# Optimization experiments

Measured on AMD Instinct MI355X. Metric: run time of the kernel, lower is better.

## Reference

```python
import jax, jax.numpy as jnp
import numpy as np

NUM_SAMPLES = 64
HIDDEN = 256
BATCH = 16384


def setup_inputs() -> dict:
    key = jax.random.key(0)
    ks = jax.random.split(key, 12)
    origins = jax.random.normal(ks[0], (BATCH, 3), dtype=jnp.float32)
    directions = jax.random.normal(ks[1], (BATCH, 3), dtype=jnp.float32)
    directions = directions / jnp.linalg.norm(directions, axis=-1, keepdims=True)

    def init_linear(k, fan_in, fan_out):
        kw, kb = jax.random.split(k)
        lim = 1.0 / np.sqrt(fan_in)
        W = jax.random.uniform(kw, (fan_in, fan_out), jnp.float32, -lim, lim)
        b = jax.random.uniform(kb, (fan_out,), jnp.float32, -lim, lim)
        return W, b

    W1, b1 = init_linear(ks[2], 3, HIDDEN)
    W2, b2 = init_linear(ks[3], HIDDEN, HIDDEN)
    W3, b3 = init_linear(ks[4], HIDDEN, HIDDEN)
    W4, b4 = init_linear(ks[5], HIDDEN, 4)
    return {
        "origins": origins, "directions": directions,
        "W1": W1, "b1": b1, "W2": W2, "b2": b2,
        "W3": W3, "b3": b3, "W4": W4, "b4": b4,
        "near": 2, "far": 6,
    }


def _field(points, W1, b1, W2, b2, W3, b3, W4, b4):
    # points: [N, 3] -> [N, 4] (rgb logits + density logit)
    h = jax.nn.relu(points @ W1 + b1)
    h = jax.nn.relu(h @ W2 + b2)
    h = jax.nn.relu(h @ W3 + b3)
    return h @ W4 + b4


def reference(origins, directions, W1, b1, W2, b2, W3, b3, W4, b4, near, far):
    near = jnp.float32(near)
    far = jnp.float32(far)
    B = origins.shape[0]
    S = NUM_SAMPLES

    # 1. Stratified (uniform midpoint) samples along each ray.
    t_vals = jnp.linspace(0.0, 1.0, S + 1, dtype=jnp.float32)      # [S+1]
    z_vals = near * (1.0 - t_vals) + far * t_vals                   # [S+1]
    boundaries = jnp.broadcast_to(z_vals, (B, S + 1))               # [B, S+1]
    z_mids = 0.5 * (z_vals[:-1] + z_vals[1:])                       # [S]
    points = origins[:, None, :] + directions[:, None, :] * z_mids[None, :, None]  # [B, S, 3]

    # 2. Evaluate field; map channels to valid ranges.
    outputs = _field(points.reshape(-1, 3), W1, b1, W2, b2, W3, b3, W4, b4)
    outputs = outputs.reshape(B, S, 4)
    emitted_radiance = jax.nn.sigmoid(outputs[..., :3])             # [B, S, 3]
    density = jax.nn.relu(outputs[..., 3])                          # [B, S]

    # 3. Alpha values from densities and segment lengths.
    deltas = boundaries[:, 1:] - boundaries[:, :-1]                 # [B, S]
    alphas = 1.0 - jnp.exp(-density * deltas)                       # [B, S]

    # 4. Alpha compositing (black background).
    trans = jnp.cumprod(
        jnp.concatenate([jnp.ones((B, 1), jnp.float32), 1.0 - alphas + 1e-10], axis=-1),
        axis=-1,
    )[:, :-1]                                                        # [B, S]
    weights = alphas * trans                                         # [B, S]
    rgb = jnp.sum(weights[..., None] * emitted_radiance, axis=1)     # [B, 3]
    return rgb
```

## Files before the change

### kernel.cpp

```cpp
#include <hip/hip_runtime.h>


#define HID 256

typedef short bf16x8 __attribute__((ext_vector_type(8)));
typedef float f32x4  __attribute__((ext_vector_type(4)));
typedef float f32x16 __attribute__((ext_vector_type(16)));
typedef int   i32x4  __attribute__((ext_vector_type(4)));
typedef int   i32x2v __attribute__((ext_vector_type(2)));

static __device__ __forceinline__ unsigned short f2bf(float f) {
    unsigned u = __float_as_uint(f);
    u += 0x7fffu + ((u >> 16) & 1u);
    return (unsigned short)(u >> 16);
}

__global__ void prep_pack(const float* __restrict__ W2, const float* __restrict__ W3,
                          const float* __restrict__ W4,
                          unsigned short* __restrict__ W2p, unsigned short* __restrict__ W3p,
                          unsigned short* __restrict__ W4p) {
    int t = blockIdx.x * 256 + threadIdx.x;
    if (t < 65536) {
        int e  = t & 7;
        int l  = (t >> 3) & 63;
        int kt = (t >> 9) & 15;
        int nt = t >> 13;
        int k = kt * 16 + 8 * (l >> 5) + e;
        int n = nt * 32 + (l & 31);
        W2p[t] = f2bf(W2[k * HID + n]);
        W3p[t] = f2bf(W3[k * HID + n]);
    } else if (t < 65536 + 8192) {
        int u  = t - 65536;
        int e  = u & 7;
        int l  = (u >> 3) & 63;
        int kt = u >> 9;
        int k = kt * 16 + 8 * (l >> 5) + e;
        int n = l & 31;
        W4p[u] = f2bf((n < 4) ? W4[k * 4 + n] : 0.0f);
    }
}

static __device__ __forceinline__ float decode_scalar(const unsigned* __restrict__ p) {
    unsigned w0 = p[0];
    if (w0 == 0u) {
        unsigned w1 = p[1];
        if (w1 != 0u) return (float)__hiloint2double((int)w1, (int)w0);
        return 0.0f;
    }
    if (w0 < 0x00800000u) return (float)(int)w0;
    return __uint_as_float(w0);
}

static __device__ __forceinline__ unsigned cvt_pk_bf16(float lo, float hi) {
    unsigned r;
    asm("v_cvt_pk_bf16_f32 %0, %1, %2" : "=v"(r) : "v"(lo), "v"(hi));
    return r;
}

static __device__ __forceinline__ void gload_lds16(const char* g, char* l) {
    __builtin_amdgcn_global_load_lds(
        (const __attribute__((address_space(1))) void*)g,
        (__attribute__((address_space(3))) void*)l, 16, 0, 0);
}

template<int BASE>
static __device__ __forceinline__ void dense_layer(
    const bf16x8 (&h)[16], bf16x8 (&o)[16], char* __restrict__ wlds,
    const char* __restrict__ W2p, const char* __restrict__ W3p,
    const char* __restrict__ W4p, const float* __restrict__ bias,
    int tid, int l, int hi)
{
#pragma unroll
    for (int st = 0; st < 8; ++st) {
        const int gi = BASE + st;
        char* live = wlds + (gi & 1) * 16384;
        char* idle = wlds + ((gi + 1) & 1) * 16384;
        const int ni = gi + 1;
        const char* nsrc = (ni < 8) ? (W2p + ni * 16384)
                         : (ni < 16 ? (W3p + (ni - 8) * 16384) : W4p);
#pragma unroll
        for (int j = 0; j < 4; ++j)
            gload_lds16(nsrc + j * 4096 + tid * 16, idle + j * 4096 + tid * 16);

        f32x16 aA = {}, aB = {};
#pragma unroll
        for (int kk = 0; kk < 16; kk += 2) {
            bf16x8 w0 = *(const bf16x8*)(live + kk * 1024 + l * 16);
            bf16x8 w1 = *(const bf16x8*)(live + (kk + 1) * 1024 + l * 16);
            aA = __builtin_amdgcn_mfma_f32_32x32x16_bf16(w0, h[kk],     aA, 0, 0, 0);
            aB = __builtin_amdgcn_mfma_f32_32x32x16_bf16(w1, h[kk + 1], aB, 0, 0, 0);
        }
        unsigned qw[4][2];
#pragma unroll
        for (int q = 0; q < 4; ++q) {
            f32x4 bb = *(const f32x4*)(bias + st * 32 + 8 * q + 4 * hi);
            float v0 = fmaxf(aA[4*q+0] + aB[4*q+0] + bb[0], 0.0f);
            float v1 = fmaxf(aA[4*q+1] + aB[4*q+1] + bb[1], 0.0f);
            float v2 = fmaxf(aA[4*q+2] + aB[4*q+2] + bb[2], 0.0f);
            float v3 = fmaxf(aA[4*q+3] + aB[4*q+3] + bb[3], 0.0f);
            qw[q][0] = cvt_pk_bf16(v0, v1);
            qw[q][1] = cvt_pk_bf16(v2, v3);
        }
#pragma unroll
        for (int j = 0; j < 2; ++j) {
            i32x2v r = __builtin_amdgcn_permlane32_swap((int)qw[0][j], (int)qw[1][j], false, false);
            i32x2v s = __builtin_amdgcn_permlane32_swap((int)qw[2][j], (int)qw[3][j], false, false);
            ((i32x4&)o[2*st  ])[j]     = r[0];
            ((i32x4&)o[2*st  ])[j + 2] = r[1];
            ((i32x4&)o[2*st+1])[j]     = s[0];
            ((i32x4&)o[2*st+1])[j + 2] = s[1];
        }
        __syncthreads();
    }
}

__launch_bounds__(256, 2)
__global__ void nerf_fused(
    const float* __restrict__ origins, const float* __restrict__ dirs,
    const float* __restrict__ W1, const float* __restrict__ b1,
    const float* __restrict__ b2, const float* __restrict__ b3,
    const float* __restrict__ b4,
    const unsigned* __restrict__ nearp, const unsigned* __restrict__ farp,
    const unsigned short* __restrict__ W2p_, const unsigned short* __restrict__ W3p_,
    const unsigned short* __restrict__ W4p_,
    float* __restrict__ out)
{
    __shared__ char wlds[32768];
    const int tid  = threadIdx.x;
    const int w    = tid >> 6;
    const int l    = tid & 63;
    const int hi   = l >> 5;
    const int half = w & 1;
    const int rloc = w >> 1;
    const long ray = (long)blockIdx.x * 2 + rloc;
    const char* W2p = (const char*)W2p_;
    const char* W3p = (const char*)W3p_;
    const char* W4p = (const char*)W4p_;

    const float nearv = decode_scalar(nearp);
    const float farv  = decode_scalar(farp);
    const float delta = (farv - nearv) * (1.0f / 64.0f);

#pragma unroll
    for (int j = 0; j < 4; ++j)
        gload_lds16(W2p + j * 4096 + tid * 16, wlds + j * 4096 + tid * 16);

    float* owdw = (float*)(wlds + 16384) + w * 512;
    {
        float o0 = origins[ray*3+0], o1 = origins[ray*3+1], o2 = origins[ray*3+2];
        float d0 = dirs[ray*3+0],    d1 = dirs[ray*3+1],    d2 = dirs[ray*3+2];
        int n0 = l * 4;
        f32x4 wa = *(const f32x4*)(W1 + n0);
        f32x4 wb = *(const f32x4*)(W1 + 256 + n0);
        f32x4 wc = *(const f32x4*)(W1 + 512 + n0);
        f32x4 bb = *(const f32x4*)(b1 + n0);
        f32x4 ow, dw;
#pragma unroll
        for (int e = 0; e < 4; ++e) {
            ow[e] = fmaf(o2, wc[e], fmaf(o1, wb[e], fmaf(o0, wa[e], bb[e])));
            dw[e] = fmaf(d2, wc[e], fmaf(d1, wb[e], d0 * wa[e]));
        }
        *(f32x4*)(owdw + n0) = ow;
        *(f32x4*)(owdw + 256 + n0) = dw;
    }
    bf16x8 hf[16], hg[16];
    {
        float s = (float)(half * 32 + (l & 31));
        float z = nearv + (farv - nearv) * (s + 0.5f) * 0.015625f;
#pragma unroll
        for (int kt = 0; kt < 16; ++kt) {
            int k0 = kt * 16 + 8 * hi;
            f32x4 oa = *(const f32x4*)(owdw + k0);
            f32x4 ob = *(const f32x4*)(owdw + k0 + 4);
            f32x4 da = *(const f32x4*)(owdw + 256 + k0);
            f32x4 db = *(const f32x4*)(owdw + 256 + k0 + 4);
            i32x4 pk;
            pk[0] = (int)cvt_pk_bf16(fmaxf(fmaf(z,da[0],oa[0]),0.f), fmaxf(fmaf(z,da[1],oa[1]),0.f));
            pk[1] = (int)cvt_pk_bf16(fmaxf(fmaf(z,da[2],oa[2]),0.f), fmaxf(fmaf(z,da[3],oa[3]),0.f));
            pk[2] = (int)cvt_pk_bf16(fmaxf(fmaf(z,db[0],ob[0]),0.f), fmaxf(fmaf(z,db[1],ob[1]),0.f));
            pk[3] = (int)cvt_pk_bf16(fmaxf(fmaf(z,db[2],ob[2]),0.f), fmaxf(fmaf(z,db[3],ob[3]),0.f));
            hf[kt] = (bf16x8&)pk;
        }
    }
    __syncthreads();

    dense_layer<0>(hf, hg, wlds, W2p, W3p, W4p, b2, tid, l, hi);
    dense_layer<8>(hg, hf, wlds, W2p, W3p, W4p, b3, tid, l, hi);

    {
        f32x16 aA = {}, aB = {};
#pragma unroll
        for (int kk = 0; kk < 16; kk += 2) {
            bf16x8 w0 = *(const bf16x8*)(wlds + kk * 1024 + l * 16);
            bf16x8 w1 = *(const bf16x8*)(wlds + (kk + 1) * 1024 + l * 16);
            aA = __builtin_amdgcn_mfma_f32_32x32x16_bf16(w0, hf[kk],     aA, 0, 0, 0);
            aB = __builtin_amdgcn_mfma_f32_32x32x16_bf16(w1, hf[kk + 1], aB, 0, 0, 0);
        }
        float* compf = (float*)(wlds + 16384);
        if (l < 32) {
            float rr = aA[0] + aB[0] + b4[0];
            float gg = aA[1] + aB[1] + b4[1];
            float bl = aA[2] + aB[2] + b4[2];
            float sg = aA[3] + aB[3] + b4[3];
            float alpha = 1.0f - __expf(-fmaxf(sg, 0.0f) * delta);
            f32x4 cv;
            cv[0] = 1.0f / (1.0f + __expf(-rr));
            cv[1] = 1.0f / (1.0f + __expf(-gg));
            cv[2] = 1.0f / (1.0f + __expf(-bl));
            cv[3] = alpha;
            *(f32x4*)(compf + (rloc * 64 + half * 32 + l) * 4) = cv;
        }
    }
    __syncthreads();

    if (w < 2) {
        const float* compf = (const float*)(wlds + 16384);
        f32x4 cv = *(const f32x4*)(compf + (w * 64 + l) * 4);
        float alpha = cv[3];
        float p = 1.0f - alpha + 1e-10f;
        float P = p;
#pragma unroll
        for (int d = 1; d < 64; d <<= 1) {
            float u = __shfl_up(P, d, 64);
            if (l >= d) P *= u;
        }
        float T = __shfl_up(P, 1, 64);
        if (l == 0) T = 1.0f;
        float wt = alpha * T;
        float cr = wt * cv[0], cg = wt * cv[1], cb = wt * cv[2];
#pragma unroll
        for (int d = 32; d >= 1; d >>= 1) {
            cr += __shfl_down(cr, d, 64);
            cg += __shfl_down(cg, d, 64);
            cb += __shfl_down(cb, d, 64);
        }
        if (l == 0) {
            long rg = (long)blockIdx.x * 2 + w;
            out[rg * 3 + 0] = cr;
            out[rg * 3 + 1] = cg;
            out[rg * 3 + 2] = cb;
        }
    }
}

extern "C" void kernel_launch(void* const* d_in, const int* in_sizes, int n_in,
                              void* d_out, int out_size, void* d_ws, size_t ws_size,
                              hipStream_t stream) {
    const float* origins = (const float*)d_in[0];
    const float* dirs    = (const float*)d_in[1];
    const float* W1 = (const float*)d_in[2];
    const float* b1 = (const float*)d_in[3];
    const float* W2 = (const float*)d_in[4];
    const float* b2 = (const float*)d_in[5];
    const float* W3 = (const float*)d_in[6];
    const float* b3 = (const float*)d_in[7];
    const float* W4 = (const float*)d_in[8];
    const float* b4 = (const float*)d_in[9];
    const unsigned* nearp = (const unsigned*)d_in[10];
    const unsigned* farp  = (const unsigned*)d_in[11];
    float* out = (float*)d_out;

    unsigned short* W2p = (unsigned short*)d_ws;
    unsigned short* W3p = W2p + 65536;
    unsigned short* W4p = W2p + 131072;

    prep_pack<<<288, 256, 0, stream>>>(W2, W3, W4, W2p, W3p, W4p);
    nerf_fused<<<8192, 256, 0, stream>>>(origins, dirs, W1, b1, b2, b3, b4,
                                         nearp, farp, W2p, W3p, W4p, out);
}
```

Baseline: 355.9 us.

## Process one full ray per wave, reusing each weight fragment across two MFMA tiles

Each wavefront now handles all 64 samples of one ray as two 32-sample tiles instead of half a ray. Every LDS weight fragment read feeds two MFMAs, which halves LDS weight traffic per sample, and the grid shrinks to 4096 blocks. Since each wave's samples stay within the wave, the compositing stage needs no block-wide sync; that barrier is replaced with a local lgkmcnt wait. The cost is doubled activation registers (two 16-entry bf16x8 arrays per buffer), which risks spilling or fewer resident waves under launch_bounds(256,2).

```diff
diff --git a/kernel.cpp b/kernel.cpp
--- a/kernel.cpp
+++ b/kernel.cpp
@@ -65,7 +65,7 @@
 
 template<int BASE>
 static __device__ __forceinline__ void dense_layer(
-    const bf16x8 (&h)[16], bf16x8 (&o)[16], char* __restrict__ wlds,
+    const bf16x8 (&h)[2][16], bf16x8 (&o)[2][16], char* __restrict__ wlds,
     const char* __restrict__ W2p, const char* __restrict__ W3p,
     const char* __restrict__ W4p, const float* __restrict__ bias,
     int tid, int l, int hi)
@@ -82,33 +82,38 @@
         for (int j = 0; j < 4; ++j)
             gload_lds16(nsrc + j * 4096 + tid * 16, idle + j * 4096 + tid * 16);
 
-        f32x16 aA = {}, aB = {};
-#pragma unroll
-        for (int kk = 0; kk < 16; kk += 2) {
-            bf16x8 w0 = *(const bf16x8*)(live + kk * 1024 + l * 16);
-            bf16x8 w1 = *(const bf16x8*)(live + (kk + 1) * 1024 + l * 16);
-            aA = __builtin_amdgcn_mfma_f32_32x32x16_bf16(w0, h[kk],     aA, 0, 0, 0);
-            aB = __builtin_amdgcn_mfma_f32_32x32x16_bf16(w1, h[kk + 1], aB, 0, 0, 0);
-        }
-        unsigned qw[4][2];
-#pragma unroll
-        for (int q = 0; q < 4; ++q) {
-            f32x4 bb = *(const f32x4*)(bias + st * 32 + 8 * q + 4 * hi);
-            float v0 = fmaxf(aA[4*q+0] + aB[4*q+0] + bb[0], 0.0f);
-            float v1 = fmaxf(aA[4*q+1] + aB[4*q+1] + bb[1], 0.0f);
-            float v2 = fmaxf(aA[4*q+2] + aB[4*q+2] + bb[2], 0.0f);
-            float v3 = fmaxf(aA[4*q+3] + aB[4*q+3] + bb[3], 0.0f);
-            qw[q][0] = cvt_pk_bf16(v0, v1);
-            qw[q][1] = cvt_pk_bf16(v2, v3);
-        }
-#pragma unroll
-        for (int j = 0; j < 2; ++j) {
-            i32x2v r = __builtin_amdgcn_permlane32_swap((int)qw[0][j], (int)qw[1][j], false, false);
-            i32x2v s = __builtin_amdgcn_permlane32_swap((int)qw[2][j], (int)qw[3][j], false, false);
-            ((i32x4&)o[2*st  ])[j]     = r[0];
-            ((i32x4&)o[2*st  ])[j + 2] = r[1];
-            ((i32x4&)o[2*st+1])[j]     = s[0];
-            ((i32x4&)o[2*st+1])[j + 2] = s[1];
+        f32x16 a0 = {}, a1 = {};
+#pragma unroll
+        for (int kk = 0; kk < 16; ++kk) {
+            bf16x8 wv = *(const bf16x8*)(live + kk * 1024 + l * 16);
+            a0 = __builtin_amdgcn_mfma_f32_32x32x16_bf16(wv, h[0][kk], a0, 0, 0, 0);
+            a1 = __builtin_amdgcn_mfma_f32_32x32x16_bf16(wv, h[1][kk], a1, 0, 0, 0);
+        }
+        f32x4 bb[4];
+#pragma unroll
+        for (int q = 0; q < 4; ++q)
+            bb[q] = *(const f32x4*)(bias + st * 32 + 8 * q + 4 * hi);
+#pragma unroll
+        for (int t = 0; t < 2; ++t) {
+            unsigned qw[4][2];
+#pragma unroll
+            for (int q = 0; q < 4; ++q) {
+                float v0 = fmaxf((t ? a1 : a0)[4*q+0] + bb[q][0], 0.0f);
+                float v1 = fmaxf((t ? a1 : a0)[4*q+1] + bb[q][1], 0.0f);
+                float v2 = fmaxf((t ? a1 : a0)[4*q+2] + bb[q][2], 0.0f);
+                float v3 = fmaxf((t ? a1 : a0)[4*q+3] + bb[q][3], 0.0f);
+                qw[q][0] = cvt_pk_bf16(v0, v1);
+                qw[q][1] = cvt_pk_bf16(v2, v3);
+            }
+#pragma unroll
+            for (int j = 0; j < 2; ++j) {
+                i32x2v r = __builtin_amdgcn_permlane32_swap((int)qw[0][j], (int)qw[1][j], false, false);
+                i32x2v s = __builtin_amdgcn_permlane32_swap((int)qw[2][j], (int)qw[3][j], false, false);
+                ((i32x4&)o[t][2*st  ])[j]     = r[0];
+                ((i32x4&)o[t][2*st  ])[j + 2] = r[1];
+                ((i32x4&)o[t][2*st+1])[j]     = s[0];
+                ((i32x4&)o[t][2*st+1])[j + 2] = s[1];
+            }
         }
         __syncthreads();
     }
@@ -130,9 +135,7 @@
     const int w    = tid >> 6;
     const int l    = tid & 63;
     const int hi   = l >> 5;
-    const int half = w & 1;
-    const int rloc = w >> 1;
-    const long ray = (long)blockIdx.x * 2 + rloc;
+    const long ray = (long)blockIdx.x * 4 + w;
     const char* W2p = (const char*)W2p_;
     const char* W3p = (const char*)W3p_;
     const char* W4p = (const char*)W4p_;
@@ -153,20 +156,21 @@
         f32x4 wa = *(const f32x4*)(W1 + n0);
         f32x4 wb = *(const f32x4*)(W1 + 256 + n0);
         f32x4 wc = *(const f32x4*)(W1 + 512 + n0);
-        f32x4 bb = *(const f32x4*)(b1 + n0);
+        f32x4 bbv = *(const f32x4*)(b1 + n0);
         f32x4 ow, dw;
 #pragma unroll
         for (int e = 0; e < 4; ++e) {
-            ow[e] = fmaf(o2, wc[e], fmaf(o1, wb[e], fmaf(o0, wa[e], bb[e])));
+            ow[e] = fmaf(o2, wc[e], fmaf(o1, wb[e], fmaf(o0, wa[e], bbv[e])));
             dw[e] = fmaf(d2, wc[e], fmaf(d1, wb[e], d0 * wa[e]));
         }
         *(f32x4*)(owdw + n0) = ow;
         *(f32x4*)(owdw + 256 + n0) = dw;
     }
-    bf16x8 hf[16], hg[16];
-    {
-        float s = (float)(half * 32 + (l & 31));
-        float z = nearv + (farv - nearv) * (s + 0.5f) * 0.015625f;
+    bf16x8 hf[2][16], hg[2][16];
+    {
+        float s0 = (float)(l & 31);
+        float z0 = nearv + (farv - nearv) * (s0 + 0.5f)  * 0.015625f;
+        float z1 = nearv + (farv - nearv) * (s0 + 32.5f) * 0.015625f;
 #pragma unroll
         for (int kt = 0; kt < 16; ++kt) {
             int k0 = kt * 16 + 8 * hi;
@@ -174,12 +178,16 @@
             f32x4 ob = *(const f32x4*)(owdw + k0 + 4);
             f32x4 da = *(const f32x4*)(owdw + 256 + k0);
             f32x4 db = *(const f32x4*)(owdw + 256 + k0 + 4);
-            i32x4 pk;
-            pk[0] = (int)cvt_pk_bf16(fmaxf(fmaf(z,da[0],oa[0]),0.f), fmaxf(fmaf(z,da[1],oa[1]),0.f));
-            pk[1] = (int)cvt_pk_bf16(fmaxf(fmaf(z,da[2],oa[2]),0.f), fmaxf(fmaf(z,da[3],oa[3]),0.f));
-            pk[2] = (int)cvt_pk_bf16(fmaxf(fmaf(z,db[0],ob[0]),0.f), fmaxf(fmaf(z,db[1],ob[1]),0.f));
-            pk[3] = (int)cvt_pk_bf16(fmaxf(fmaf(z,db[2],ob[2]),0.f), fmaxf(fmaf(z,db[3],ob[3]),0.f));
-            hf[kt] = (bf16x8&)pk;
+#pragma unroll
+            for (int t = 0; t < 2; ++t) {
+                float z = t ? z1 : z0;
+                i32x4 pk;
+                pk[0] = (int)cvt_pk_bf16(fmaxf(fmaf(z,da[0],oa[0]),0.f), fmaxf(fmaf(z,da[1],oa[1]),0.f));
+                pk[1] = (int)cvt_pk_bf16(fmaxf(fmaf(z,da[2],oa[2]),0.f), fmaxf(fmaf(z,da[3],oa[3]),0.f));
+                pk[2] = (int)cvt_pk_bf16(fmaxf(fmaf(z,db[0],ob[0]),0.f), fmaxf(fmaf(z,db[1],ob[1]),0.f));
+                pk[3] = (int)cvt_pk_bf16(fmaxf(fmaf(z,db[2],ob[2]),0.f), fmaxf(fmaf(z,db[3],ob[3]),0.f));
+                hf[t][kt] = (bf16x8&)pk;
+            }
         }
     }
     __syncthreads();
@@ -187,35 +195,37 @@
     dense_layer<0>(hf, hg, wlds, W2p, W3p, W4p, b2, tid, l, hi);
     dense_layer<8>(hg, hf, wlds, W2p, W3p, W4p, b3, tid, l, hi);
 
-    {
-        f32x16 aA = {}, aB = {};
-#pragma unroll
-        for (int kk = 0; kk < 16; kk += 2) {
-            bf16x8 w0 = *(const bf16x8*)(wlds + kk * 1024 + l * 16);
-            bf16x8 w1 = *(const bf16x8*)(wlds + (kk + 1) * 1024 + l * 16);
-            aA = __builtin_amdgcn_mfma_f32_32x32x16_bf16(w0, hf[kk],     aA, 0, 0, 0);
-            aB = __builtin_amdgcn_mfma_f32_32x32x16_bf16(w1, hf[kk + 1], aB, 0, 0, 0);
-        }
-        float* compf = (float*)(wlds + 16384);
+    float* comp = (float*)(wlds + 16384);
+    {
+        f32x16 a0 = {}, a1 = {};
+#pragma unroll
+        for (int kk = 0; kk < 16; ++kk) {
+            bf16x8 wv = *(const bf16x8*)(wlds + kk * 1024 + l * 16);
+            a0 = __builtin_amdgcn_mfma_f32_32x32x16_bf16(wv, hf[0][kk], a0, 0, 0, 0);
+            a1 = __builtin_amdgcn_mfma_f32_32x32x16_bf16(wv, hf[1][kk], a1, 0, 0, 0);
+        }
         if (l < 32) {
-            float rr = aA[0] + aB[0] + b4[0];
-            float gg = aA[1] + aB[1] + b4[1];
-            float bl = aA[2] + aB[2] + b4[2];
-            float sg = aA[3] + aB[3] + b4[3];
-            float alpha = 1.0f - __expf(-fmaxf(sg, 0.0f) * delta);
-            f32x4 cv;
-            cv[0] = 1.0f / (1.0f + __expf(-rr));
-            cv[1] = 1.0f / (1.0f + __expf(-gg));
-            cv[2] = 1.0f / (1.0f + __expf(-bl));
-            cv[3] = alpha;
-            *(f32x4*)(compf + (rloc * 64 + half * 32 + l) * 4) = cv;
-        }
-    }
-    __syncthreads();
-
-    if (w < 2) {
-        const float* compf = (const float*)(wlds + 16384);
-        f32x4 cv = *(const f32x4*)(compf + (w * 64 + l) * 4);
+            float bb0 = b4[0], bb1 = b4[1], bb2 = b4[2], bb3 = b4[3];
+#pragma unroll
+            for (int t = 0; t < 2; ++t) {
+                float rr = (t ? a1 : a0)[0] + bb0;
+                float gg = (t ? a1 : a0)[1] + bb1;
+                float bl = (t ? a1 : a0)[2] + bb2;
+                float sg = (t ? a1 : a0)[3] + bb3;
+                float alpha = 1.0f - __expf(-fmaxf(sg, 0.0f) * delta);
+                f32x4 cv;
+                cv[0] = 1.0f / (1.0f + __expf(-rr));
+                cv[1] = 1.0f / (1.0f + __expf(-gg));
+                cv[2] = 1.0f / (1.0f + __expf(-bl));
+                cv[3] = alpha;
+                *(f32x4*)(comp + (w * 64 + t * 32 + l) * 4) = cv;
+            }
+        }
+        asm volatile("s_waitcnt lgkmcnt(0)" ::: "memory");
+    }
+
+    {
+        f32x4 cv = *(const f32x4*)(comp + (w * 64 + l) * 4);
         float alpha = cv[3];
         float p = 1.0f - alpha + 1e-10f;
         float P = p;
@@ -235,10 +245,9 @@
             cb += __shfl_down(cb, d, 64);
         }
         if (l == 0) {
-            long rg = (long)blockIdx.x * 2 + w;
-            out[rg * 3 + 0] = cr;
-            out[rg * 3 + 1] = cg;
-            out[rg * 3 + 2] = cb;
+            out[ray * 3 + 0] = cr;
+            out[ray * 3 + 1] = cg;
+            out[ray * 3 + 2] = cb;
         }
     }
 }
@@ -265,6 +274,6 @@
     unsigned short* W4p = W2p + 131072;
 
     prep_pack<<<288, 256, 0, stream>>>(W2, W3, W4, W2p, W3p, W4p);
-    nerf_fused<<<8192, 256, 0, stream>>>(origins, dirs, W1, b1, b2, b3, b4,
+    nerf_fused<<<4096, 256, 0, stream>>>(origins, dirs, W1, b1, b2, b3, b4,
                                          nearp, farp, W2p, W3p, W4p, out);
 }
```

After: 480.9 us. 1.35x slower.
